# Kernel optimization log

Hardware: AMD Instinct MI355X
Metric: run time of the kernel (lower is better)

## Reference

```python
import jax, jax.numpy as jnp
import numpy as np

EPS = 1e-8  # torch F.cosine_similarity eps


def setup_inputs() -> dict:
    key = jax.random.key(0)
    ks = jax.random.split(key, 5)
    S, Q, D_in, D, N_WAY, K_SHOT = 100, 4096, 21168, 64, 20, 5
    return {
        "support_images": jax.random.normal(ks[0], (S, D_in), dtype=jnp.float32),
        "support_labels": jax.random.randint(ks[1], (S,), 0, N_WAY),
        "query_images": jax.random.normal(ks[2], (Q, D_in), dtype=jnp.float32),
        "n_way": N_WAY,
        "k_shot": K_SHOT,
        "backbone_w": jax.random.normal(ks[3], (D_in, D), dtype=jnp.float32) * 0.02,
        "backbone_b": jax.random.normal(ks[4], (D,), dtype=jnp.float32) * 0.02,
    }


def _l2_normalize(x):
    # matches torch cosine_similarity: x / max(||x||, eps)
    n = jnp.maximum(jnp.linalg.norm(x, axis=-1, keepdims=True), EPS)
    return x / n


def reference(support_images, support_labels, query_images, n_way, k_shot,
              backbone_w, backbone_b):
    # Backbone: linear embedding (stand-in for conv feature extractor)
    support_emb = support_images @ backbone_w + backbone_b   # [S, D]
    query_emb = query_images @ backbone_w + backbone_b       # [Q, D]

    # Cosine similarity between every query and every support sample: [Q, S]
    sims = _l2_normalize(query_emb) @ _l2_normalize(support_emb).T

    # Softmax over the support axis (per query), as in the original loop
    attn = jax.nn.softmax(sims, axis=1)                      # [Q, S]

    # Per-label scatter-add == one-hot segment-sum: [Q, n_way]
    one_hot = jax.nn.one_hot(support_labels, n_way, dtype=attn.dtype)  # [S, n_way]
    logits = attn @ one_hot
    return logits
```

## Files before the change

kernel.cpp:

```cpp
#include <hip/hip_runtime.h>
#include <hip/hip_bf16.h>
#include <math.h>

#define DEMB 64
#define BM   64
#define BKF  64
#define KSMAX 32

using short8 = __attribute__((ext_vector_type(8))) short;
using u16x8  = __attribute__((ext_vector_type(8))) unsigned short;
using f32x4  = __attribute__((ext_vector_type(4))) float;

__device__ __forceinline__ u16x8 cvt_bf8(float4 a0, float4 a1) {
    union { u16x8 s; __hip_bfloat16 h[8]; } u;
    u.h[0] = __float2bfloat16(a0.x);
    u.h[1] = __float2bfloat16(a0.y);
    u.h[2] = __float2bfloat16(a0.z);
    u.h[3] = __float2bfloat16(a0.w);
    u.h[4] = __float2bfloat16(a1.x);
    u.h[5] = __float2bfloat16(a1.y);
    u.h[6] = __float2bfloat16(a1.z);
    u.h[7] = __float2bfloat16(a1.w);
    return u.s;
}

__device__ __forceinline__ void gl16(const void* gsrc, void* lds) {
    __builtin_amdgcn_global_load_lds(
        (const __attribute__((address_space(1))) unsigned int*)gsrc,
        (__attribute__((address_space(3))) unsigned int*)lds,
        16, 0, 0);
}

__global__ __launch_bounds__(256) void prep_wt(
    const float* __restrict__ W, unsigned short* __restrict__ Wtk, int Din)
{
    const int t = blockIdx.x * 256 + threadIdx.x;
    const int oct = t >> 6, c = t & 63;
    union { u16x8 v; __hip_bfloat16 h[8]; } u;
    #pragma unroll
    for (int j = 0; j < 8; ++j) {
        int k = oct * 8 + j;
        float x = (k < Din) ? W[(size_t)k * DEMB + c] : 0.f;
        u.h[j] = __float2bfloat16(x);
    }
    *reinterpret_cast<u16x8*>(&Wtk[(size_t)t * 8]) = u.v;
}

__global__ __launch_bounds__(256) void gemm_mfma(
    const float* __restrict__ Xq, const float* __restrict__ Xs,
    const unsigned short* __restrict__ Wtk,
    float* __restrict__ qpart, float* __restrict__ spart,
    int Q, int S, int Din, int nQb, int cpk, int nbatch)
{
    __shared__ float          As[2][BM * BKF];
    __shared__ unsigned short Bs[2][8 * 64 * 8];

    const int tid  = threadIdx.x;
    const int wave = tid >> 6;
    const int lane = tid & 63;
    const int kg   = blockIdx.y;

    const bool isS = (int)blockIdx.x >= nQb;
    const float* X = isS ? Xs : Xq;
    const int nrows = isS ? S : Q;
    const int r0 = (isS ? ((int)blockIdx.x - nQb) : (int)blockIdx.x) * BM;
    float* part = isS ? spart : qpart;
    const int prow = isS ? 128 : Q;

    const int g  = lane >> 4;
    const int qp = lane & 15;

    const int col16 = lane & 15;
    const int frow  = 16 * wave + col16;
    const int fk    = (lane >> 4) * 8;

    f32x4 acc[4] = { {0.f,0.f,0.f,0.f}, {0.f,0.f,0.f,0.f},
                     {0.f,0.f,0.f,0.f}, {0.f,0.f,0.f,0.f} };

    const int b0 = kg * cpk;
    int b1 = b0 + cpk; if (b1 > nbatch) b1 = nbatch;

#define STAGE(P, B) do {                                                       \
    const int kb_ = (B) * BKF;                                                 \
    _Pragma("unroll")                                                          \
    for (int i = 0; i < 4; ++i) {                                              \
        int rg_ = r0 + 16 * wave + 4 * i + g;                                  \
        if (rg_ >= nrows) rg_ = nrows - 1;                                     \
        const int q_ = qp ^ (4 * i + g);                                       \
        int kq_ = kb_ + 4 * q_;                                                \
        if (kq_ >= Din) kq_ = 0;                                               \
        gl16(X + (size_t)rg_ * Din + kq_,                                      \
             &As[P][(16 * wave + 4 * i) * BKF]);                               \
    }                                                                          \
    _Pragma("unroll")                                                          \
    for (int j = 0; j < 2; ++j) {                                              \
        gl16(Wtk + ((size_t)((B) * 8 + 2 * wave + j) * 64 + lane) * 8,         \
             &Bs[P][(2 * wave + j) * 512]);                                    \
    }                                                                          \
} while (0)

#define COMPUTE(P, CC) do {                                                    \
    const int qa_ = (CC) * 8 + (fk >> 2);                                      \
    const float* Ab_ = &As[P][frow * BKF];                                     \
    float4 fa_ = *reinterpret_cast<const float4*>(Ab_ + ((qa_    ) ^ col16) * 4); \
    float4 fb_ = *reinterpret_cast<const float4*>(Ab_ + ((qa_ + 1) ^ col16) * 4); \
    u16x8 afu_ = cvt_bf8(fa_, fb_);                                            \
    short8 af_ = (short8)afu_;                                                 \
    const int ob_ = ((CC) * 4 + (fk >> 3)) * 64;                               \
    short8 b0_ = *reinterpret_cast<const short8*>(&Bs[P][(ob_ +  0 + col16) * 8]); \
    short8 b1_ = *reinterpret_cast<const short8*>(&Bs[P][(ob_ + 16 + col16) * 8]); \
    short8 b2_ = *reinterpret_cast<const short8*>(&Bs[P][(ob_ + 32 + col16) * 8]); \
    short8 b3_ = *reinterpret_cast<const short8*>(&Bs[P][(ob_ + 48 + col16) * 8]); \
    acc[0] = __builtin_amdgcn_mfma_f32_16x16x32_bf16(af_, b0_, acc[0], 0, 0, 0);  \
    acc[1] = __builtin_amdgcn_mfma_f32_16x16x32_bf16(af_, b1_, acc[1], 0, 0, 0);  \
    acc[2] = __builtin_amdgcn_mfma_f32_16x16x32_bf16(af_, b2_, acc[2], 0, 0, 0);  \
    acc[3] = __builtin_amdgcn_mfma_f32_16x16x32_bf16(af_, b3_, acc[3], 0, 0, 0);  \
} while (0)

    STAGE(0, b0);
    __syncthreads();

    int cur = 0;
    for (int b = b0; b < b1; ++b) {
        if (b + 1 < b1) STAGE(cur ^ 1, b + 1);
        COMPUTE(cur, 0);
        COMPUTE(cur, 1);
        __syncthreads();
        cur ^= 1;
    }

#undef STAGE
#undef COMPUTE

    #pragma unroll
    for (int cb = 0; cb < 4; ++cb) {
        #pragma unroll
        for (int i = 0; i < 4; ++i) {
            int row = r0 + 16 * wave + (lane >> 4) * 4 + i;
            if (row < nrows)
                part[((size_t)kg * prow + row) * DEMB + 16 * cb + col16] = acc[cb][i];
        }
    }
}

__global__ void support_finalize(const float* __restrict__ spart,
                                 const float* __restrict__ bias,
                                 float* __restrict__ sn, int S, int nkg)
{
    int s = blockIdx.x;
    int c = threadIdx.x;
    float e = bias[c];
    for (int g = 0; g < nkg; ++g)
        e += spart[((size_t)g * 128 + s) * DEMB + c];
    float ss = e * e;
    #pragma unroll
    for (int o = 32; o >= 1; o >>= 1) ss += __shfl_xor(ss, o, 64);
    sn[(size_t)s * DEMB + c] = e / fmaxf(sqrtf(ss), 1e-8f);
}

__global__ __launch_bounds__(256) void attend(
    const float* __restrict__ qpart, const float* __restrict__ sn_g,
    const float* __restrict__ bias, const int* __restrict__ labels,
    const int* __restrict__ p_nway, float* __restrict__ out,
    int S, int Q, int nkg)
{
    __shared__ float sn[100][65];
    __shared__ float qn[4][64];
    __shared__ float bins[4][32];
    __shared__ int   lab[100];

    const int tid  = threadIdx.x;
    const int w    = tid >> 6;
    const int lane = tid & 63;
    const int nw   = *p_nway;

    for (int i = tid; i < S * DEMB; i += 256) sn[i >> 6][i & 63] = sn_g[i];
    if (tid < S) lab[tid] = labels[tid];

    const int q = blockIdx.x * 4 + w;

    float e = bias[lane];
    for (int g = 0; g < nkg; ++g)
        e += qpart[((size_t)g * Q + q) * DEMB + lane];
    float ss = e * e;
    #pragma unroll
    for (int o = 32; o >= 1; o >>= 1) ss += __shfl_xor(ss, o, 64);
    e /= fmaxf(sqrtf(ss), 1e-8f);
    qn[w][lane] = e;
    if (lane < 32) bins[w][lane] = 0.f;
    __syncthreads();

    const bool v1 = (lane + 64) < S;
    const int  s1 = v1 ? lane + 64 : 0;
    float sim0 = 0.f, sim1 = 0.f;
    #pragma unroll 8
    for (int c = 0; c < DEMB; ++c) {
        float qc = qn[w][c];
        sim0 += qc * sn[lane][c];
        sim1 += qc * sn[s1][c];
    }
    if (!v1) sim1 = -INFINITY;

    float lm = fmaxf(sim0, sim1);
    #pragma unroll
    for (int o = 32; o >= 1; o >>= 1) lm = fmaxf(lm, __shfl_xor(lm, o, 64));
    float e0 = __expf(sim0 - lm);
    float e1 = v1 ? __expf(sim1 - lm) : 0.f;
    float d = e0 + e1;
    #pragma unroll
    for (int o = 32; o >= 1; o >>= 1) d += __shfl_xor(d, o, 64);

    atomicAdd(&bins[w][lab[lane]], e0);
    if (v1) atomicAdd(&bins[w][lab[s1]], e1);
    __syncthreads();

    if (lane < nw) out[(size_t)q * nw + lane] = bins[w][lane] / d;
}

extern "C" void kernel_launch(void* const* d_in, const int* in_sizes, int n_in,
                              void* d_out, int out_size, void* d_ws, size_t ws_size,
                              hipStream_t stream)
{
    const float* sup    = (const float*)d_in[0];
    const int*   labels = (const int*)d_in[1];
    const float* qry    = (const float*)d_in[2];
    const int*   p_nway = (const int*)d_in[3];
    const float* W      = (const float*)d_in[5];
    const float* bias   = (const float*)d_in[6];
    float* out = (float*)d_out;

    const int D   = DEMB;
    const int Din = in_sizes[5] / D;
    const int Q   = in_sizes[2] / Din;
    const int S   = in_sizes[1];

    const int nbatch = (Din + BKF - 1) / BKF;
    const int Koct   = nbatch * 8;

    char* wsb = (char*)d_ws;
    size_t wt_bytes = (size_t)Koct * 64 * 16;
    wt_bytes = (wt_bytes + 255) & ~(size_t)255;
    size_t sn_bytes = (size_t)S * D * sizeof(float);
    sn_bytes = (sn_bytes + 255) & ~(size_t)255;
    size_t per_ks = ((size_t)Q * D + 128 * D) * sizeof(float);

    size_t fixed = wt_bytes + sn_bytes;
    int ks = 1;
    if (ws_size > fixed + per_ks) {
        size_t avail = (ws_size - fixed) / per_ks;
        ks = (int)(avail < KSMAX ? avail : KSMAX);
        if (ks < 1) ks = 1;
    }
    const int cpk = (nbatch + ks - 1) / ks;
    const int nkg = (nbatch + cpk - 1) / cpk;

    unsigned short* Wtk = (unsigned short*)wsb;
    float* sn    = (float*)(wsb + wt_bytes);
    float* spart = (float*)(wsb + wt_bytes + sn_bytes);
    float* qpart = spart + (size_t)nkg * 128 * D;

    hipLaunchKernelGGL(prep_wt, dim3((Koct * 64) / 256), dim3(256), 0, stream,
                       W, Wtk, Din);

    const int nQb = (Q + BM - 1) / BM;
    const int nSb = (S + BM - 1) / BM;
    hipLaunchKernelGGL(gemm_mfma, dim3(nQb + nSb, nkg), dim3(256), 0, stream,
                       qry, sup, Wtk, qpart, spart, Q, S, Din, nQb, cpk, nbatch);

    hipLaunchKernelGGL(support_finalize, dim3(S), dim3(64), 0, stream,
                       spart, bias, sn, S, nkg);

    hipLaunchKernelGGL(attend, dim3(Q / 4), dim3(256), 0, stream,
                       qpart, sn, bias, labels, p_nway, out, S, Q, nkg);
}
```

Before: 119.8 us.

## Triple-buffer GEMM staging with explicit vmcnt waits and single barrier

Moves the backbone GEMM from double to triple buffering of the A and B LDS tiles, so loads run two k-batches ahead of compute. Synchronisation now uses an explicit s_waitcnt on outstanding vector memory ops (allowing the newest stage's six loads to stay in flight) followed by one barrier per iteration, replacing the syncthreads after compute. KSMAX is also halved, which changes how the k dimension is split across blocks and the partial-sum count. Triple buffering raises LDS per block by about half, which may reduce occupancy, and the hand-coded vmcnt count assumes exactly six loads per stage.

```diff
diff --git a/kernel.cpp b/kernel.cpp
--- a/kernel.cpp
+++ b/kernel.cpp
@@ -5,7 +5,7 @@
 #define DEMB 64
 #define BM   64
 #define BKF  64
-#define KSMAX 32
+#define KSMAX 16
 
 using short8 = __attribute__((ext_vector_type(8))) short;
 using u16x8  = __attribute__((ext_vector_type(8))) unsigned short;
@@ -52,8 +52,8 @@
     float* __restrict__ qpart, float* __restrict__ spart,
     int Q, int S, int Din, int nQb, int cpk, int nbatch)
 {
-    __shared__ float          As[2][BM * BKF];
-    __shared__ unsigned short Bs[2][8 * 64 * 8];
+    __shared__ float          As[3][BM * BKF];
+    __shared__ unsigned short Bs[3][8 * 64 * 8];
 
     const int tid  = threadIdx.x;
     const int wave = tid >> 6;
@@ -80,7 +80,7 @@
     const int b0 = kg * cpk;
     int b1 = b0 + cpk; if (b1 > nbatch) b1 = nbatch;
 
-#define STAGE(P, B) do {                                                       \
+#define STAGE(SL, B) do {                                                      \
     const int kb_ = (B) * BKF;                                                 \
     _Pragma("unroll")                                                          \
     for (int i = 0; i < 4; ++i) {                                              \
@@ -90,27 +90,27 @@
         int kq_ = kb_ + 4 * q_;                                                \
         if (kq_ >= Din) kq_ = 0;                                               \
         gl16(X + (size_t)rg_ * Din + kq_,                                      \
-             &As[P][(16 * wave + 4 * i) * BKF]);                               \
+             &As[SL][(16 * wave + 4 * i) * BKF]);                              \
     }                                                                          \
     _Pragma("unroll")                                                          \
     for (int j = 0; j < 2; ++j) {                                              \
         gl16(Wtk + ((size_t)((B) * 8 + 2 * wave + j) * 64 + lane) * 8,         \
-             &Bs[P][(2 * wave + j) * 512]);                                    \
+             &Bs[SL][(2 * wave + j) * 512]);                                   \
     }                                                                          \
 } while (0)
 
-#define COMPUTE(P, CC) do {                                                    \
+#define COMPUTE(SL, CC) do {                                                   \
     const int qa_ = (CC) * 8 + (fk >> 2);                                      \
-    const float* Ab_ = &As[P][frow * BKF];                                     \
+    const float* Ab_ = &As[SL][frow * BKF];                                    \
     float4 fa_ = *reinterpret_cast<const float4*>(Ab_ + ((qa_    ) ^ col16) * 4); \
     float4 fb_ = *reinterpret_cast<const float4*>(Ab_ + ((qa_ + 1) ^ col16) * 4); \
     u16x8 afu_ = cvt_bf8(fa_, fb_);                                            \
     short8 af_ = (short8)afu_;                                                 \
     const int ob_ = ((CC) * 4 + (fk >> 3)) * 64;                               \
-    short8 b0_ = *reinterpret_cast<const short8*>(&Bs[P][(ob_ +  0 + col16) * 8]); \
-    short8 b1_ = *reinterpret_cast<const short8*>(&Bs[P][(ob_ + 16 + col16) * 8]); \
-    short8 b2_ = *reinterpret_cast<const short8*>(&Bs[P][(ob_ + 32 + col16) * 8]); \
-    short8 b3_ = *reinterpret_cast<const short8*>(&Bs[P][(ob_ + 48 + col16) * 8]); \
+    short8 b0_ = *reinterpret_cast<const short8*>(&Bs[SL][(ob_ +  0 + col16) * 8]); \
+    short8 b1_ = *reinterpret_cast<const short8*>(&Bs[SL][(ob_ + 16 + col16) * 8]); \
+    short8 b2_ = *reinterpret_cast<const short8*>(&Bs[SL][(ob_ + 32 + col16) * 8]); \
+    short8 b3_ = *reinterpret_cast<const short8*>(&Bs[SL][(ob_ + 48 + col16) * 8]); \
     acc[0] = __builtin_amdgcn_mfma_f32_16x16x32_bf16(af_, b0_, acc[0], 0, 0, 0);  \
     acc[1] = __builtin_amdgcn_mfma_f32_16x16x32_bf16(af_, b1_, acc[1], 0, 0, 0);  \
     acc[2] = __builtin_amdgcn_mfma_f32_16x16x32_bf16(af_, b2_, acc[2], 0, 0, 0);  \
@@ -118,15 +118,18 @@
 } while (0)
 
     STAGE(0, b0);
-    __syncthreads();
-
-    int cur = 0;
+    if (b0 + 1 < b1) STAGE(1, b0 + 1);
+
     for (int b = b0; b < b1; ++b) {
-        if (b + 1 < b1) STAGE(cur ^ 1, b + 1);
-        COMPUTE(cur, 0);
-        COMPUTE(cur, 1);
-        __syncthreads();
-        cur ^= 1;
+        if (b + 1 < b1) asm volatile("s_waitcnt vmcnt(6)" ::: "memory");
+        else            asm volatile("s_waitcnt vmcnt(0)" ::: "memory");
+        __builtin_amdgcn_s_barrier();
+
+        const int sl = (b - b0) % 3;
+        if (b + 2 < b1) STAGE((sl + 2) % 3, b + 2);
+
+        COMPUTE(sl, 0);
+        COMPUTE(sl, 1);
     }
 
 #undef STAGE
```

After: 117.7 us. About the same (-1.7%).
